# Kernel tuning notes

Measured on AMD Instinct MI355X. Metric: run time of the kernel, lower is better.

## Reference

```python
import jax, jax.numpy as jnp
import numpy as np

N_USERS = 10000
N_ITEMS = 40000
HID = 64
NNZ = 2_000_000
B = 8192
N_TOT = N_USERS + N_ITEMS
HOP = 3


def setup_inputs() -> dict:
    key = jax.random.key(0)
    ks = jax.random.split(key, 13)
    emb = lambda k, n: jax.random.normal(k, (n, HID), dtype=jnp.float32) * (1.0 / np.sqrt(HID))
    # Dense social adjacency; scaled so repeated propagation stays numerically stable
    S = jax.random.uniform(ks[6], (N_USERS, N_USERS), dtype=jnp.float32) * (2.0 / N_USERS)
    return {
        "users": jax.random.randint(ks[0], (B,), 0, N_USERS),
        "pos": jax.random.randint(ks[1], (B,), 0, N_ITEMS),
        "neg": jax.random.randint(ks[2], (B,), 0, N_ITEMS),
        "user_embs": emb(ks[3], N_USERS),
        "item_embs": emb(ks[4], N_ITEMS),
        "user1_embs": emb(ks[5], N_USERS),
        "item1_embs": emb(ks[7], N_ITEMS),
        "user2_embs": emb(ks[8], N_USERS),
        "item2_embs": emb(ks[9], N_ITEMS),
        "S": S,
        "A_rows": jax.random.randint(ks[10], (NNZ,), 0, N_TOT, dtype=jnp.int32),
        "A_cols": jax.random.randint(ks[11], (NNZ,), 0, N_TOT, dtype=jnp.int32),
        "A_vals": jax.random.uniform(ks[12], (NNZ,), dtype=jnp.float32) * (1.0 / 40.0),
        "hop": HOP,
    }


def social_gcn(uemb, S, hop):
    # LightGCN-style propagation over dense social graph; mean over layers 0..hop
    h = uemb
    acc = uemb
    for _ in range(hop):
        h = S @ h                      # [n_users, hid] dense GEMM
        acc = acc + h
    return acc / (hop + 1)


def ui_gcn(uemb, iemb, rows, cols, vals, hop):
    # LightGCN over sparse bipartite user-item graph of size [N_TOT, N_TOT]
    ego = jnp.concatenate([uemb, iemb], axis=0)   # [N_TOT, hid]
    h = ego
    acc = ego
    for _ in range(hop):
        msgs = vals[:, None] * h[cols]            # gather + scale  [nnz, hid]
        h = jax.ops.segment_sum(msgs, rows, num_segments=N_TOT)
        acc = acc + h
    out = acc / (hop + 1)
    return out[:N_USERS], out[N_USERS:]


def reference(users, pos, neg, user_embs, item_embs, user1_embs, item1_embs,
              user2_embs, item2_embs, S, A_rows, A_cols, A_vals, hop):
    all_user_S = social_gcn(user_embs, S, hop)
    all_user_A, all_item = ui_gcn(user_embs, item_embs, A_rows, A_cols, A_vals, hop)
    all_user = 0.5 * all_user_S + 0.5 * all_user_A

    all_user_social = social_gcn(user1_embs, S, hop)
    all_item_social = item1_embs
    all_user_rating, all_item_rating = ui_gcn(user2_embs, item2_embs, A_rows, A_cols, A_vals, hop)

    return (all_user[users], all_item[pos], all_item[neg],
            all_user_S, all_user_A,
            all_user_social[users], all_item_social[pos], all_item_social[neg],
            all_user_rating[users], all_item_rating[pos], all_item_rating[neg])
```

## Files before the change

kernel.cpp:

```cpp
#include <hip/hip_runtime.h>

#define N_USERS 10000
#define N_ITEMS 40000
#define N_TOTAL 50000
#define HID     64
#define BATCH   8192
#define HOPS    3
#define KDIM    10000
#define KTILES  157
#define KPAD    (KTILES * 64)
#define MTILES  79
#define SPLITK  8
#define NSOC    (MTILES * SPLITK)
#define CP_STRIDE ((size_t)MTILES * 16384)

#define O0 0
#define O1 524288
#define O2 1048576
#define O3 1572864
#define O4 2212864
#define O5 2852864
#define O6 3377152
#define O7 3901440
#define O8 4425728
#define O9 4950016
#define O10 5474304

typedef __attribute__((ext_vector_type(8))) short short8;
typedef __attribute__((ext_vector_type(4))) float floatx4;

__device__ __forceinline__ unsigned short f32bf(float f) {
  union { float f; unsigned u; } v; v.f = f;
  unsigned r = v.u + 0x7fffu + ((v.u >> 16) & 1u);
  return (unsigned short)(r >> 16);
}

__device__ __forceinline__ unsigned packbf2(float x, float y) {
  return (unsigned)f32bf(x) | ((unsigned)f32bf(y) << 16);
}

__device__ __forceinline__ short8 cvt8(floatx4 v0, floatx4 v1) {
  short8 o;
  o[0] = (short)f32bf(v0[0]); o[1] = (short)f32bf(v0[1]);
  o[2] = (short)f32bf(v0[2]); o[3] = (short)f32bf(v0[3]);
  o[4] = (short)f32bf(v1[0]); o[5] = (short)f32bf(v1[1]);
  o[6] = (short)f32bf(v1[2]); o[7] = (short)f32bf(v1[3]);
  return o;
}

__global__ __launch_bounds__(256)
void init_all(const float* __restrict__ ue, const float* __restrict__ u1,
              const float* __restrict__ ie, const float* __restrict__ u2,
              const float* __restrict__ i2, const int* __restrict__ Arows,
              int* __restrict__ counts, int nnz,
              float* __restrict__ HS0, float* __restrict__ HSacc,
              unsigned* __restrict__ Eb0, float* __restrict__ Eacc) {
  int b = blockIdx.x, t = threadIdx.x;
  if (b < 2500) {
    int i = b * 256 + t;
    int r = i >> 6, c = i & 63;
    float a = ue[i], x = u1[i];
    size_t p = (size_t)r * 128 + c;
    HS0[p] = a; HS0[p + 64] = x;
    HSacc[p] = a; HSacc[p + 64] = x;
  } else if (b < 8750) {
    int i = (b - 2500) * 256 + t;
    int r = i >> 5, c2 = (i & 31) * 2;
    const float* srcA; const float* srcB;
    if (r < N_USERS) { srcA = ue + (size_t)r * 64 + c2; srcB = u2 + (size_t)r * 64 + c2; }
    else { srcA = ie + (size_t)(r - N_USERS) * 64 + c2; srcB = i2 + (size_t)(r - N_USERS) * 64 + c2; }
    float2 a = *(const float2*)srcA;
    float2 x = *(const float2*)srcB;
    size_t p = (size_t)r * 128 + c2;
    *(float2*)&Eacc[p] = a;
    *(float2*)&Eacc[p + 64] = x;
    Eb0[(size_t)r * 64 + (c2 >> 1)] = packbf2(a.x, a.y);
    Eb0[(size_t)r * 64 + 32 + (c2 >> 1)] = packbf2(x.x, x.y);
  } else {
    int i = (b - 8750) * 256 + t;
    if (i < nnz) atomicAdd(&counts[Arows[i]], 1);
  }
}

__global__ void scan1(const int* __restrict__ counts, int* __restrict__ offs, int* __restrict__ bsum) {
  __shared__ int sh[256];
  int t = threadIdx.x;
  int base = blockIdx.x * 1024 + t * 4;
  int v0 = 0, v1 = 0, v2 = 0, v3 = 0;
  if (base + 0 < N_TOTAL) v0 = counts[base + 0];
  if (base + 1 < N_TOTAL) v1 = counts[base + 1];
  if (base + 2 < N_TOTAL) v2 = counts[base + 2];
  if (base + 3 < N_TOTAL) v3 = counts[base + 3];
  int s = v0 + v1 + v2 + v3;
  sh[t] = s;
  __syncthreads();
  for (int d = 1; d < 256; d <<= 1) {
    int x = (t >= d) ? sh[t - d] : 0;
    __syncthreads();
    sh[t] += x;
    __syncthreads();
  }
  int excl = sh[t] - s;
  if (t == 255) bsum[blockIdx.x] = sh[255];
  if (base + 0 < N_TOTAL) offs[base + 0] = excl; excl += v0;
  if (base + 1 < N_TOTAL) offs[base + 1] = excl; excl += v1;
  if (base + 2 < N_TOTAL) offs[base + 2] = excl; excl += v2;
  if (base + 3 < N_TOTAL) offs[base + 3] = excl;
}

__global__ void scan2(int* __restrict__ bsum, int nb) {
  __shared__ int sh[64];
  int t = threadIdx.x;
  int v = (t < nb) ? bsum[t] : 0;
  sh[t] = v;
  __syncthreads();
  for (int d = 1; d < 64; d <<= 1) {
    int x = (t >= d) ? sh[t - d] : 0;
    __syncthreads();
    sh[t] += x;
    __syncthreads();
  }
  if (t < nb) bsum[t] = sh[t] - v;
}

__device__ __forceinline__ void bfrag_emit(int t, const float* __restrict__ ts,
                                           unsigned short* __restrict__ Bf) {
  int tid = threadIdx.x;
#pragma unroll
  for (int i = 0; i < 4; i++) {
    int c0 = tid + i * 256;
    int nt = c0 >> 7, kk = (c0 >> 6) & 1, l = c0 & 63;
    int quad = l >> 4, mq = l & 15;
    short8 o;
#pragma unroll
    for (int j = 0; j < 8; j++)
      o[j] = (short)f32bf(ts[(kk * 32 + quad * 8 + j) * 132 + nt * 16 + mq]);
    *(short8*)&Bf[(((size_t)t * 8 + nt) * 2 + kk) * 512 + l * 8] = o;
  }
}

__device__ __forceinline__ void bfrag_from_h(int t, const float* __restrict__ H,
                                             unsigned short* __restrict__ Bf,
                                             float* __restrict__ ts) {
  int k0 = t * 64;
  int tid = threadIdx.x;
#pragma unroll
  for (int i = 0; i < 8; i++) {
    int f = tid + i * 256;
    int r = f >> 5, c4 = (f & 31) * 4;
    float4 v = make_float4(0.f, 0.f, 0.f, 0.f);
    if (k0 + r < KDIM) v = *(const float4*)&H[(size_t)(k0 + r) * 128 + c4];
    *(float4*)&ts[r * 132 + c4] = v;
  }
  __syncthreads();
  bfrag_emit(t, ts, Bf);
}

__device__ __forceinline__ void bfrag_from_parts(int t, const float* __restrict__ Cpart,
                                                 unsigned short* __restrict__ Bf,
                                                 float* __restrict__ ts) {
  int k0 = t * 64;
  int tid = threadIdx.x;
#pragma unroll
  for (int i = 0; i < 8; i++) {
    int f = tid + i * 256;
    int r = f >> 5, c4 = (f & 31) * 4;
    float4 v = make_float4(0.f, 0.f, 0.f, 0.f);
    int gk = k0 + r;
    if (gk < KDIM) {
      const float* p = Cpart + (size_t)(gk >> 7) * 16384 + (size_t)(gk & 127) * 128 + c4;
#pragma unroll
      for (int ks = 0; ks < SPLITK; ks++) {
        float4 q = *(const float4*)p; p += CP_STRIDE;
        v.x += q.x; v.y += q.y; v.z += q.z; v.w += q.w;
      }
    }
    *(float4*)&ts[r * 132 + c4] = v;
  }
  __syncthreads();
  bfrag_emit(t, ts, Bf);
}

__global__ __launch_bounds__(256)
void scan3_bf(int* __restrict__ offs, const int* __restrict__ bexcl,
              int* __restrict__ cursor, int nnz,
              const float* __restrict__ hc, unsigned short* __restrict__ Bf) {
  __shared__ __align__(16) float ts[64 * 132];
  if (blockIdx.x < 196) {
    int i = blockIdx.x * 256 + threadIdx.x;
    if (i < N_TOTAL) {
      int v = offs[i] + bexcl[i >> 10];
      offs[i] = v; cursor[i] = v;
    }
    if (i == 0) offs[N_TOTAL] = nnz;
  } else {
    bfrag_from_h(blockIdx.x - 196, hc, Bf, ts);
  }
}

__global__ void scatter_csr(const int* __restrict__ rows, const int* __restrict__ cols,
                            const float* __restrict__ vals, int* __restrict__ cursor,
                            int2* __restrict__ edges, int n) {
  int i = blockIdx.x * 256 + threadIdx.x;
  if (i < n) {
    int p = atomicAdd(&cursor[rows[i]], 1);
    edges[p] = make_int2(cols[i], __float_as_int(vals[i]));
  }
}

template<int FIRST>
__global__ __launch_bounds__(256)
void social_gemm(const float* __restrict__ S, unsigned short* __restrict__ Sbf,
                 const unsigned short* __restrict__ Bf, float* __restrict__ Cpart) {
  int tid = threadIdx.x;
  int w = tid >> 6, lane = tid & 63;
  int quad = lane >> 4, mq = lane & 15;
  int mtile = blockIdx.x % MTILES;
  int ks = blockIdx.x / MTILES;
  int m0 = mtile * 128;
  int t0 = (ks * KTILES) / SPLITK;
  int t1 = ((ks + 1) * KTILES) / SPLITK;

  floatx4 acc[2][8];
#pragma unroll
  for (int rf = 0; rf < 2; rf++)
#pragma unroll
    for (int nt = 0; nt < 8; nt++) acc[rf][nt] = (floatx4){0.f, 0.f, 0.f, 0.f};

  int r0 = m0 + w * 32 + mq;
  int r1 = r0 + 16;
  const float* sr0 = S + (size_t)r0 * KDIM;
  const float* sr1 = S + (size_t)r1 * KDIM;
  size_t sb = (((size_t)mtile * KTILES) * 8 + w * 2) * 1024 + (size_t)lane * 8;

#pragma unroll 2
  for (int t = t0; t < t1; ++t) {
    short8 a00, a01, a10, a11;
    size_t st = sb + (size_t)t * 8192;
    if (FIRST) {
      int kb = t * 64 + quad * 8;
      a00 = a01 = a10 = a11 = (short8){0, 0, 0, 0, 0, 0, 0, 0};
      {
        int k = kb;
        if (r0 < KDIM && k < KDIM)
          a00 = cvt8(__builtin_nontemporal_load((const floatx4*)(sr0 + k)),
                     __builtin_nontemporal_load((const floatx4*)(sr0 + k + 4)));
        k = kb + 32;
        if (r0 < KDIM && k < KDIM)
          a01 = cvt8(__builtin_nontemporal_load((const floatx4*)(sr0 + k)),
                     __builtin_nontemporal_load((const floatx4*)(sr0 + k + 4)));
        k = kb;
        if (r1 < KDIM && k < KDIM)
          a10 = cvt8(__builtin_nontemporal_load((const floatx4*)(sr1 + k)),
                     __builtin_nontemporal_load((const floatx4*)(sr1 + k + 4)));
        k = kb + 32;
        if (r1 < KDIM && k < KDIM)
          a11 = cvt8(__builtin_nontemporal_load((const floatx4*)(sr1 + k)),
                     __builtin_nontemporal_load((const floatx4*)(sr1 + k + 4)));
      }
      *(short8*)&Sbf[st]        = a00;
      *(short8*)&Sbf[st + 512]  = a01;
      *(short8*)&Sbf[st + 1024] = a10;
      *(short8*)&Sbf[st + 1536] = a11;
    } else {
      a00 = *(const short8*)&Sbf[st];
      a01 = *(const short8*)&Sbf[st + 512];
      a10 = *(const short8*)&Sbf[st + 1024];
      a11 = *(const short8*)&Sbf[st + 1536];
    }
    const unsigned short* bfb = Bf + (size_t)t * 8192 + lane * 8;
#pragma unroll
    for (int kk = 0; kk < 2; kk++) {
      short8 b[8];
#pragma unroll
      for (int nt = 0; nt < 8; nt++)
        b[nt] = *(const short8*)&bfb[((size_t)nt * 2 + kk) * 512];
      short8 ax0 = kk ? a01 : a00;
      short8 ax1 = kk ? a11 : a10;
#pragma unroll
      for (int nt = 0; nt < 8; nt++) {
        acc[0][nt] = __builtin_amdgcn_mfma_f32_16x16x32_bf16(ax0, b[nt], acc[0][nt], 0, 0, 0);
        acc[1][nt] = __builtin_amdgcn_mfma_f32_16x16x32_bf16(ax1, b[nt], acc[1][nt], 0, 0, 0);
      }
    }
  }
  float* cp = Cpart + ((size_t)ks * MTILES + mtile) * 16384;
#pragma unroll
  for (int rf = 0; rf < 2; rf++) {
#pragma unroll
    for (int nt = 0; nt < 8; nt++) {
      int col = nt * 16 + mq;
      int rb = w * 32 + rf * 16 + quad * 4;
#pragma unroll
      for (int i = 0; i < 4; i++)
        cp[(size_t)(rb + i) * 128 + col] = acc[rf][nt][i];
    }
  }
}

template<int LAST>
__global__ __launch_bounds__(256)
void ui_hop(const int* __restrict__ offs, const int2* __restrict__ edges,
            const unsigned* __restrict__ Ebin, unsigned* __restrict__ Ebout,
            float* __restrict__ Eacc) {
  int wid = blockIdx.x * 4 + (threadIdx.x >> 6);
  int lane = threadIdx.x & 63;
  const unsigned* Einl = Ebin + lane;
  int s = offs[wid], e = offs[wid + 1];
  float ax = 0.f, ay = 0.f;
  int j = s;
  for (; j + 4 <= e; j += 4) {
    int2 e0 = edges[j], e1 = edges[j + 1], e2 = edges[j + 2], e3 = edges[j + 3];
    unsigned u0 = Einl[(size_t)e0.x * 64];
    unsigned u1 = Einl[(size_t)e1.x * 64];
    unsigned u2 = Einl[(size_t)e2.x * 64];
    unsigned u3 = Einl[(size_t)e3.x * 64];
    float w0 = __int_as_float(e0.y), w1 = __int_as_float(e1.y);
    float w2 = __int_as_float(e2.y), w3 = __int_as_float(e3.y);
    ax += w0 * __uint_as_float(u0 << 16) + w1 * __uint_as_float(u1 << 16)
        + w2 * __uint_as_float(u2 << 16) + w3 * __uint_as_float(u3 << 16);
    ay += w0 * __uint_as_float(u0 & 0xffff0000u) + w1 * __uint_as_float(u1 & 0xffff0000u)
        + w2 * __uint_as_float(u2 & 0xffff0000u) + w3 * __uint_as_float(u3 & 0xffff0000u);
  }
  for (; j < e; ++j) {
    int2 ed = edges[j];
    unsigned u = Einl[(size_t)ed.x * 64];
    float w = __int_as_float(ed.y);
    ax += w * __uint_as_float(u << 16);
    ay += w * __uint_as_float(u & 0xffff0000u);
  }
  if (!LAST) Ebout[(size_t)wid * 64 + lane] = packbf2(ax, ay);
  size_t op = (size_t)wid * 128 + lane * 2;
  float2 a = *(float2*)&Eacc[op];
  a.x += ax; a.y += ay;
  *(float2*)&Eacc[op] = a;
}

__global__ __launch_bounds__(256)
void prep_kernel(const float* __restrict__ Cpart, unsigned short* __restrict__ Bf,
                 float* __restrict__ HSacc) {
  __shared__ __align__(16) float ts[64 * 132];
  if (blockIdx.x < KTILES) {
    bfrag_from_parts(blockIdx.x, Cpart, Bf, ts);
  } else {
    int i = (blockIdx.x - KTILES) * 256 + threadIdx.x;
    if (i < (N_USERS * 128) / 4) {
      int r = i >> 5, c = (i & 31) * 4;
      const float* p = Cpart + (size_t)(r >> 7) * 16384 + (size_t)(r & 127) * 128 + c;
      float4 v = make_float4(0.f, 0.f, 0.f, 0.f);
#pragma unroll
      for (int ks = 0; ks < SPLITK; ks++) {
        float4 q = *(const float4*)p; p += CP_STRIDE;
        v.x += q.x; v.y += q.y; v.z += q.z; v.w += q.w;
      }
      float4 a = ((float4*)HSacc)[i];
      a.x += v.x; a.y += v.y; a.z += v.z; a.w += v.w;
      ((float4*)HSacc)[i] = a;
    }
  }
}

__global__ __launch_bounds__(256)
void reduce2(const float* __restrict__ Cpart, float* __restrict__ HSacc) {
  int i = blockIdx.x * 256 + threadIdx.x;
  if (i < (N_USERS * 128) / 4) {
    int r = i >> 5, c = (i & 31) * 4;
    const float* p = Cpart + (size_t)(r >> 7) * 16384 + (size_t)(r & 127) * 128 + c;
    float4 v = make_float4(0.f, 0.f, 0.f, 0.f);
#pragma unroll
    for (int ks = 0; ks < SPLITK; ks++) {
      float4 q = *(const float4*)p; p += CP_STRIDE;
      v.x += q.x; v.y += q.y; v.z += q.z; v.w += q.w;
    }
    float4 a = ((float4*)HSacc)[i];
    a.x += v.x; a.y += v.y; a.z += v.z; a.w += v.w;
    ((float4*)HSacc)[i] = a;
  }
}

__global__ __launch_bounds__(256)
void out_kernel(const int* __restrict__ users, const int* __restrict__ pos,
                const int* __restrict__ neg, const float* __restrict__ HSacc,
                const float* __restrict__ Eacc, const float* __restrict__ item1,
                float* __restrict__ out) {
  if (blockIdx.x < 2500) {
    int i = blockIdx.x * 256 + threadIdx.x;
    int r = i >> 6, c = i & 63;
    out[O3 + i] = HSacc[(size_t)r * 128 + c] * 0.25f;
    out[O4 + i] = Eacc[(size_t)r * 128 + c] * 0.25f;
  } else {
    int b = (blockIdx.x - 2500) * 4 + (threadIdx.x >> 6);
    int lane = threadIdx.x & 63;
    int u = users[b], p = pos[b], n = neg[b];
    const float q = 0.25f;
    float us = HSacc[(size_t)u * 128 + lane] * q;
    float ua = Eacc[(size_t)u * 128 + lane] * q;
    size_t bl = (size_t)b * 64 + lane;
    out[O0 + bl]  = 0.5f * (us + ua);
    out[O1 + bl]  = Eacc[(size_t)(N_USERS + p) * 128 + lane] * q;
    out[O2 + bl]  = Eacc[(size_t)(N_USERS + n) * 128 + lane] * q;
    out[O5 + bl]  = HSacc[(size_t)u * 128 + 64 + lane] * q;
    out[O6 + bl]  = item1[(size_t)p * 64 + lane];
    out[O7 + bl]  = item1[(size_t)n * 64 + lane];
    out[O8 + bl]  = Eacc[(size_t)u * 128 + 64 + lane] * q;
    out[O9 + bl]  = Eacc[(size_t)(N_USERS + p) * 128 + 64 + lane] * q;
    out[O10 + bl] = Eacc[(size_t)(N_USERS + n) * 128 + 64 + lane] * q;
  }
}

extern "C" void kernel_launch(void* const* d_in, const int* in_sizes, int n_in,
                              void* d_out, int out_size, void* d_ws, size_t ws_size,
                              hipStream_t stream) {
  (void)n_in; (void)out_size; (void)ws_size;
  const int*   users = (const int*)d_in[0];
  const int*   pos   = (const int*)d_in[1];
  const int*   neg   = (const int*)d_in[2];
  const float* ue    = (const float*)d_in[3];
  const float* ie    = (const float*)d_in[4];
  const float* u1    = (const float*)d_in[5];
  const float* i1    = (const float*)d_in[6];
  const float* u2    = (const float*)d_in[7];
  const float* i2    = (const float*)d_in[8];
  const float* S     = (const float*)d_in[9];
  const int*   Arows = (const int*)d_in[10];
  const int*   Acols = (const int*)d_in[11];
  const float* Avals = (const float*)d_in[12];
  const int nnz = in_sizes[10];

  char* ws = (char*)d_ws;
  size_t off = 0;
  auto alloc = [&](size_t b) { size_t r = off; off += (b + 255) & ~(size_t)255; return r; };
  float* HS0   = (float*)(ws + alloc(sizeof(float) * (size_t)N_USERS * 128));
  float* HSacc = (float*)(ws + alloc(sizeof(float) * (size_t)N_USERS * 128));
  unsigned short* Bf  = (unsigned short*)(ws + alloc(sizeof(short) * (size_t)KTILES * 8192));
  unsigned short* Sbf = (unsigned short*)(ws + alloc(sizeof(short) * (size_t)MTILES * KTILES * 8192));
  float* Cpart = (float*)(ws + alloc(sizeof(float) * (size_t)SPLITK * CP_STRIDE));
  unsigned* Eb0 = (unsigned*)(ws + alloc(sizeof(unsigned) * (size_t)N_TOTAL * 64));
  unsigned* Eb1 = (unsigned*)(ws + alloc(sizeof(unsigned) * (size_t)N_TOTAL * 64));
  float* Eacc  = (float*)(ws + alloc(sizeof(float) * (size_t)N_TOTAL * 128));
  int* counts  = (int*)(ws + alloc(sizeof(int) * (N_TOTAL + 16)));
  int* offs    = (int*)(ws + alloc(sizeof(int) * (N_TOTAL + 16)));
  int* cursor  = (int*)(ws + alloc(sizeof(int) * (N_TOTAL + 16)));
  int* bsum    = (int*)(ws + alloc(sizeof(int) * 256));
  int2* edges  = (int2*)(ws + alloc(sizeof(int2) * (size_t)nnz));

  const int histB = (nnz + 255) / 256;

  hipMemsetAsync(counts, 0, sizeof(int) * (N_TOTAL + 16), stream);
  init_all<<<8750 + histB, 256, 0, stream>>>(ue, u1, ie, u2, i2, Arows, counts, nnz,
                                             HS0, HSacc, Eb0, Eacc);
  scan1<<<49, 256, 0, stream>>>(counts, offs, bsum);
  scan2<<<1, 64, 0, stream>>>(bsum, 49);
  scan3_bf<<<196 + KTILES, 256, 0, stream>>>(offs, bsum, cursor, nnz, HS0, Bf);
  scatter_csr<<<histB, 256, 0, stream>>>(Arows, Acols, Avals, cursor, edges, nnz);

  ui_hop<0><<<12500, 256, 0, stream>>>(offs, edges, Eb0, Eb1, Eacc);
  social_gemm<1><<<NSOC, 256, 0, stream>>>(S, Sbf, Bf, Cpart);
  prep_kernel<<<KTILES + 1250, 256, 0, stream>>>(Cpart, Bf, HSacc);
  ui_hop<0><<<12500, 256, 0, stream>>>(offs, edges, Eb1, Eb0, Eacc);
  social_gemm<0><<<NSOC, 256, 0, stream>>>(S, Sbf, Bf, Cpart);
  prep_kernel<<<KTILES + 1250, 256, 0, stream>>>(Cpart, Bf, HSacc);
  ui_hop<1><<<12500, 256, 0, stream>>>(offs, edges, Eb0, Eb1, Eacc);
  social_gemm<0><<<NSOC, 256, 0, stream>>>(S, Sbf, Bf, Cpart);
  reduce2<<<1250, 256, 0, stream>>>(Cpart, HSacc);

  float* out = (float*)d_out;
  out_kernel<<<2500 + 2048, 256, 0, stream>>>(users, pos, neg, HSacc, Eacc, i1, out);
}
```

Before: 1.386 ms.

## Co-schedule UI sparse hops with social GEMM and prep in fused launches

Independent work is merged into shared grids: the first UI hop runs alongside the first social GEMM, and later UI hops run in the same launch as the split-K reduction and bf16 fragment preparation. This removes launch gaps and lets the memory-bound sparse gather overlap with GEMM and reduction work. The fragment builder now stages 16 rows at a time, cutting shared memory from about 33KB to about 8KB so the fused prep/UI kernel keeps UI-block occupancy, at the cost of extra barriers. A heavier fused kernel could suffer register or occupancy pressure from the merged code paths.

```diff
diff --git a/kernel.cpp b/kernel.cpp
--- a/kernel.cpp
+++ b/kernel.cpp
@@ -13,6 +13,8 @@
 #define SPLITK  8
 #define NSOC    (MTILES * SPLITK)
 #define CP_STRIDE ((size_t)MTILES * 16384)
+#define UIBLK   12500
+#define REDBLK  1250
 
 #define O0 0
 #define O1 524288
@@ -123,69 +125,75 @@
   if (t < nb) bsum[t] = sh[t] - v;
 }
 
-__device__ __forceinline__ void bfrag_emit(int t, const float* __restrict__ ts,
-                                           unsigned short* __restrict__ Bf) {
+__device__ __forceinline__ void bfrag16_emit(int t, int s, const float* __restrict__ ts,
+                                             unsigned short* __restrict__ Bf) {
   int tid = threadIdx.x;
-#pragma unroll
-  for (int i = 0; i < 4; i++) {
-    int c0 = tid + i * 256;
-    int nt = c0 >> 7, kk = (c0 >> 6) & 1, l = c0 & 63;
-    int quad = l >> 4, mq = l & 15;
-    short8 o;
-#pragma unroll
-    for (int j = 0; j < 8; j++)
-      o[j] = (short)f32bf(ts[(kk * 32 + quad * 8 + j) * 132 + nt * 16 + mq]);
-    *(short8*)&Bf[(((size_t)t * 8 + nt) * 2 + kk) * 512 + l * 8] = o;
-  }
-}
-
-__device__ __forceinline__ void bfrag_from_h(int t, const float* __restrict__ H,
-                                             unsigned short* __restrict__ Bf,
-                                             float* __restrict__ ts) {
-  int k0 = t * 64;
+  int nt = tid >> 5, l31 = tid & 31;
+  int lane = (s & 1) * 32 + l31;
+  int mq = lane & 15, q1 = (lane >> 4) & 1;
+  int kk = s >> 1;
+  short8 o;
+#pragma unroll
+  for (int j = 0; j < 8; j++)
+    o[j] = (short)f32bf(ts[(q1 * 8 + j) * 132 + nt * 16 + mq]);
+  *(short8*)&Bf[(((size_t)t * 8 + nt) * 2 + kk) * 512 + lane * 8] = o;
+}
+
+__device__ __forceinline__ void bfrag16_from_h(int t, const float* __restrict__ H,
+                                               unsigned short* __restrict__ Bf,
+                                               float* __restrict__ ts) {
   int tid = threadIdx.x;
 #pragma unroll
-  for (int i = 0; i < 8; i++) {
-    int f = tid + i * 256;
-    int r = f >> 5, c4 = (f & 31) * 4;
-    float4 v = make_float4(0.f, 0.f, 0.f, 0.f);
-    if (k0 + r < KDIM) v = *(const float4*)&H[(size_t)(k0 + r) * 128 + c4];
-    *(float4*)&ts[r * 132 + c4] = v;
-  }
-  __syncthreads();
-  bfrag_emit(t, ts, Bf);
-}
-
-__device__ __forceinline__ void bfrag_from_parts(int t, const float* __restrict__ Cpart,
-                                                 unsigned short* __restrict__ Bf,
-                                                 float* __restrict__ ts) {
-  int k0 = t * 64;
+  for (int s = 0; s < 4; s++) {
+    int k0 = t * 64 + s * 16;
+#pragma unroll
+    for (int i = 0; i < 2; i++) {
+      int f = tid + i * 256;
+      int r = f >> 5, c4 = (f & 31) * 4;
+      float4 v = make_float4(0.f, 0.f, 0.f, 0.f);
+      if (k0 + r < KDIM) v = *(const float4*)&H[(size_t)(k0 + r) * 128 + c4];
+      *(float4*)&ts[r * 132 + c4] = v;
+    }
+    __syncthreads();
+    bfrag16_emit(t, s, ts, Bf);
+    __syncthreads();
+  }
+}
+
+__device__ __forceinline__ void bfrag16_from_parts(int t, const float* __restrict__ Cpart,
+                                                   unsigned short* __restrict__ Bf,
+                                                   float* __restrict__ ts) {
   int tid = threadIdx.x;
 #pragma unroll
-  for (int i = 0; i < 8; i++) {
-    int f = tid + i * 256;
-    int r = f >> 5, c4 = (f & 31) * 4;
-    float4 v = make_float4(0.f, 0.f, 0.f, 0.f);
-    int gk = k0 + r;
-    if (gk < KDIM) {
-      const float* p = Cpart + (size_t)(gk >> 7) * 16384 + (size_t)(gk & 127) * 128 + c4;
-#pragma unroll
-      for (int ks = 0; ks < SPLITK; ks++) {
-        float4 q = *(const float4*)p; p += CP_STRIDE;
-        v.x += q.x; v.y += q.y; v.z += q.z; v.w += q.w;
+  for (int s = 0; s < 4; s++) {
+    int k0 = t * 64 + s * 16;
+#pragma unroll
+    for (int i = 0; i < 2; i++) {
+      int f = tid + i * 256;
+      int r = f >> 5, c4 = (f & 31) * 4;
+      float4 v = make_float4(0.f, 0.f, 0.f, 0.f);
+      int gk = k0 + r;
+      if (gk < KDIM) {
+        const float* p = Cpart + (size_t)(gk >> 7) * 16384 + (size_t)(gk & 127) * 128 + c4;
+#pragma unroll
+        for (int ks = 0; ks < SPLITK; ks++) {
+          float4 q = *(const float4*)p; p += CP_STRIDE;
+          v.x += q.x; v.y += q.y; v.z += q.z; v.w += q.w;
+        }
       }
-    }
-    *(float4*)&ts[r * 132 + c4] = v;
-  }
-  __syncthreads();
-  bfrag_emit(t, ts, Bf);
+      *(float4*)&ts[r * 132 + c4] = v;
+    }
+    __syncthreads();
+    bfrag16_emit(t, s, ts, Bf);
+    __syncthreads();
+  }
 }
 
 __global__ __launch_bounds__(256)
 void scan3_bf(int* __restrict__ offs, const int* __restrict__ bexcl,
               int* __restrict__ cursor, int nnz,
               const float* __restrict__ hc, unsigned short* __restrict__ Bf) {
-  __shared__ __align__(16) float ts[64 * 132];
+  __shared__ __align__(16) float ts[16 * 132];
   if (blockIdx.x < 196) {
     int i = blockIdx.x * 256 + threadIdx.x;
     if (i < N_TOTAL) {
@@ -194,7 +202,7 @@
     }
     if (i == 0) offs[N_TOTAL] = nnz;
   } else {
-    bfrag_from_h(blockIdx.x - 196, hc, Bf, ts);
+    bfrag16_from_h(blockIdx.x - 196, hc, Bf, ts);
   }
 }
 
@@ -209,14 +217,15 @@
 }
 
 template<int FIRST>
-__global__ __launch_bounds__(256)
-void social_gemm(const float* __restrict__ S, unsigned short* __restrict__ Sbf,
-                 const unsigned short* __restrict__ Bf, float* __restrict__ Cpart) {
+__device__ __forceinline__ void gemm_body(int bid, const float* __restrict__ S,
+                                          unsigned short* __restrict__ Sbf,
+                                          const unsigned short* __restrict__ Bf,
+                                          float* __restrict__ Cpart) {
   int tid = threadIdx.x;
   int w = tid >> 6, lane = tid & 63;
   int quad = lane >> 4, mq = lane & 15;
-  int mtile = blockIdx.x % MTILES;
-  int ks = blockIdx.x / MTILES;
+  int mtile = bid % MTILES;
+  int ks = bid / MTILES;
   int m0 = mtile * 128;
   int t0 = (ks * KTILES) / SPLITK;
   int t1 = ((ks + 1) * KTILES) / SPLITK;
@@ -299,11 +308,12 @@
 }
 
 template<int LAST>
-__global__ __launch_bounds__(256)
-void ui_hop(const int* __restrict__ offs, const int2* __restrict__ edges,
-            const unsigned* __restrict__ Ebin, unsigned* __restrict__ Ebout,
-            float* __restrict__ Eacc) {
-  int wid = blockIdx.x * 4 + (threadIdx.x >> 6);
+__device__ __forceinline__ void ui_body(int rb, const int* __restrict__ offs,
+                                        const int2* __restrict__ edges,
+                                        const unsigned* __restrict__ Ebin,
+                                        unsigned* __restrict__ Ebout,
+                                        float* __restrict__ Eacc) {
+  int wid = rb * 4 + (threadIdx.x >> 6);
   int lane = threadIdx.x & 63;
   const unsigned* Einl = Ebin + lane;
   int s = offs[wid], e = offs[wid + 1];
@@ -337,13 +347,30 @@
 }
 
 __global__ __launch_bounds__(256)
-void prep_kernel(const float* __restrict__ Cpart, unsigned short* __restrict__ Bf,
-                 float* __restrict__ HSacc) {
-  __shared__ __align__(16) float ts[64 * 132];
-  if (blockIdx.x < KTILES) {
-    bfrag_from_parts(blockIdx.x, Cpart, Bf, ts);
+void hop0_fused(const float* __restrict__ S, unsigned short* __restrict__ Sbf,
+                const unsigned short* __restrict__ Bf, float* __restrict__ Cpart,
+                const int* __restrict__ offs, const int2* __restrict__ edges,
+                const unsigned* __restrict__ Eb0, unsigned* __restrict__ Eb1,
+                float* __restrict__ Eacc) {
+  if (blockIdx.x < NSOC) gemm_body<1>(blockIdx.x, S, Sbf, Bf, Cpart);
+  else ui_body<0>(blockIdx.x - NSOC, offs, edges, Eb0, Eb1, Eacc);
+}
+
+template<int LAST>
+__global__ __launch_bounds__(256)
+void prep_ui(const float* __restrict__ Cpart, unsigned short* __restrict__ Bf,
+             float* __restrict__ HSacc,
+             const int* __restrict__ offs, const int2* __restrict__ edges,
+             const unsigned* __restrict__ Ebin, unsigned* __restrict__ Ebout,
+             float* __restrict__ Eacc) {
+  __shared__ __align__(16) float ts[16 * 132];
+  int b = blockIdx.x;
+  if (b < UIBLK) {
+    ui_body<LAST>(b, offs, edges, Ebin, Ebout, Eacc);
+  } else if (b < UIBLK + KTILES) {
+    bfrag16_from_parts(b - UIBLK, Cpart, Bf, ts);
   } else {
-    int i = (blockIdx.x - KTILES) * 256 + threadIdx.x;
+    int i = (b - UIBLK - KTILES) * 256 + threadIdx.x;
     if (i < (N_USERS * 128) / 4) {
       int r = i >> 5, c = (i & 31) * 4;
       const float* p = Cpart + (size_t)(r >> 7) * 16384 + (size_t)(r & 127) * 128 + c;
@@ -358,6 +385,12 @@
       ((float4*)HSacc)[i] = a;
     }
   }
+}
+
+__global__ __launch_bounds__(256)
+void social_gemm(const float* __restrict__ S, unsigned short* __restrict__ Sbf,
+                 const unsigned short* __restrict__ Bf, float* __restrict__ Cpart) {
+  gemm_body<0>(blockIdx.x, S, Sbf, Bf, Cpart);
 }
 
 __global__ __launch_bounds__(256)
@@ -454,15 +487,14 @@
   scan3_bf<<<196 + KTILES, 256, 0, stream>>>(offs, bsum, cursor, nnz, HS0, Bf);
   scatter_csr<<<histB, 256, 0, stream>>>(Arows, Acols, Avals, cursor, edges, nnz);
 
-  ui_hop<0><<<12500, 256, 0, stream>>>(offs, edges, Eb0, Eb1, Eacc);
-  social_gemm<1><<<NSOC, 256, 0, stream>>>(S, Sbf, Bf, Cpart);
-  prep_kernel<<<KTILES + 1250, 256, 0, stream>>>(Cpart, Bf, HSacc);
-  ui_hop<0><<<12500, 256, 0, stream>>>(offs, edges, Eb1, Eb0, Eacc);
-  social_gemm<0><<<NSOC, 256, 0, stream>>>(S, Sbf, Bf, Cpart);
-  prep_kernel<<<KTILES + 1250, 256, 0, stream>>>(Cpart, Bf, HSacc);
-  ui_hop<1><<<12500, 256, 0, stream>>>(offs, edges, Eb0, Eb1, Eacc);
-  social_gemm<0><<<NSOC, 256, 0, stream>>>(S, Sbf, Bf, Cpart);
-  reduce2<<<1250, 256, 0, stream>>>(Cpart, HSacc);
+  hop0_fused<<<NSOC + UIBLK, 256, 0, stream>>>(S, Sbf, Bf, Cpart, offs, edges, Eb0, Eb1, Eacc);
+  prep_ui<0><<<UIBLK + KTILES + REDBLK, 256, 0, stream>>>(Cpart, Bf, HSacc,
+                                                          offs, edges, Eb1, Eb0, Eacc);
+  social_gemm<<<NSOC, 256, 0, stream>>>(S, Sbf, Bf, Cpart);
+  prep_ui<1><<<UIBLK + KTILES + REDBLK, 256, 0, stream>>>(Cpart, Bf, HSacc,
+                                                          offs, edges, Eb0, Eb1, Eacc);
+  social_gemm<<<NSOC, 256, 0, stream>>>(S, Sbf, Bf, Cpart);
+  reduce2<<<REDBLK, 256, 0, stream>>>(Cpart, HSacc);
 
   float* out = (float*)d_out;
   out_kernel<<<2500 + 2048, 256, 0, stream>>>(users, pos, neg, HSacc, Eacc, i1, out);
```

Result: no change. 1.411 ms (+1.8%).
